# Kernel optimization log

Measured on AMD Instinct MI355X. Metric: run time of the kernel, lower is better.

Reference implementation:

```python
import jax, jax.numpy as jnp
import numpy as np

B = 256
N = 256


def setup_inputs() -> dict:
    key = jax.random.key(0)
    ks = jax.random.split(key, 6)
    X = jax.random.normal(ks[0], (B, N), dtype=jnp.float32)
    context = jax.random.normal(ks[1], (B, N), dtype=jnp.float32)
    W = jax.random.normal(ks[2], (N, N), dtype=jnp.float32) * 0.1
    scale = jnp.ones((1,), dtype=jnp.float32)
    A = jax.random.uniform(ks[3], (N, N), dtype=jnp.float32)
    cl_weight = jax.random.normal(ks[4], (N * N, N), dtype=jnp.float32) * 0.02
    cl_bias = jax.random.normal(ks[5], (N * N,), dtype=jnp.float32) * 0.02
    t = 3
    return {"X": X, "context": context, "W": W, "scale": scale, "A": A,
            "cl_weight": cl_weight, "cl_bias": cl_bias, "t": t}


def reference(X, context, W, scale, A, cl_weight, cl_bias, t):
    # context_L path: context-conditioned adjustment of W, shape [B, N, N]
    Bsz, n = X.shape
    adjust = (context @ cl_weight.T + cl_bias).reshape(Bsz, n, n)
    W_new = adjust + W  # broadcast [N,N] over batch
    # diag term: sum over rows i of (W_new @ A)[b, i, k] = einsum bij,jk->bk
    d = jnp.einsum('bij,jk->bk', W_new, A)
    eye = jnp.eye(n, dtype=X.dtype)
    L = d[:, :, None] * eye - W_new          # diag_embed(d) - W_new, [B,N,N]
    new_context = context * (t / (t + 1)) + X / (t + 1)
    L_T = scale * jnp.swapaxes(L, -1, -2)    # [B,N,N]
    update = jnp.einsum('bn,bnm->bm', X, L_T)  # matmul(X[...,None,:], L_T).squeeze()
    return (update, new_context)
```

## Files before the change

### kernel.cpp

```cpp
#include <hip/hip_runtime.h>

#define N 256
#define NN 65536

typedef __attribute__((ext_vector_type(8))) __bf16 bf16x8;
typedef __attribute__((ext_vector_type(4))) __bf16 bf16x4v;
typedef __attribute__((ext_vector_type(4))) float f32x4;

#define F_PART   0u
#define F_CSPART 2097152u
#define F_WSC    3145728u
#define F_CSB    3145984u
#define F_SFULL  3178752u
#define F_YADJ   3244288u
#define WS_FLOATS 3309824u

static __device__ __forceinline__ f32x4 mfma16(bf16x8 a, bf16x8 b, f32x4 c) {
  return __builtin_amdgcn_mfma_f32_16x16x32_bf16(a, b, c, 0, 0, 0);
}
static __device__ __forceinline__ bf16x4v pack4(float4 v) {
  bf16x4v r;
  r[0] = (__bf16)v.x; r[1] = (__bf16)v.y; r[2] = (__bf16)v.z; r[3] = (__bf16)v.w;
  return r;
}
static __device__ __forceinline__ bf16x8 pack8(float4 a, float4 b) {
  bf16x8 r;
  r[0] = (__bf16)a.x; r[1] = (__bf16)a.y; r[2] = (__bf16)a.z; r[3] = (__bf16)a.w;
  r[4] = (__bf16)b.x; r[5] = (__bf16)b.y; r[6] = (__bf16)b.z; r[7] = (__bf16)b.w;
  return r;
}

__global__ void __launch_bounds__(512) kbig(
    const float* __restrict__ X, const float* __restrict__ ctx,
    const float* __restrict__ W, const float* __restrict__ clb,
    const float* __restrict__ clw, float* __restrict__ ws)
{
  extern __shared__ char smem[];
  float* xl  = (float*)(smem + 65536);
  float* red = (float*)smem;
  const int t = threadIdx.x;
  const int mg = blockIdx.x >> 5, s = blockIdx.x & 31;
  const int m0 = mg * 16, n0 = s * 8;

  const int lane = t & 63, w = t >> 6;
  const int wb = w * 32;
  const int l15 = lane & 15, lhi = lane >> 4;
  const float4* clwf4 = (const float4*)clw;

  bf16x8 af[2][8];
#pragma unroll
  for (int i = 0; i < 2; ++i)
#pragma unroll
    for (int c = 0; c < 8; ++c) {
      const float4* p = (const float4*)(ctx + (wb + i * 16 + l15) * N +
                                        c * 32 + lhi * 8);
      af[i][c] = pack8(p[0], p[1]);
    }
  if (t < 256) {
    const float4* xp = (const float4*)(X + t * N + n0);
    const float4 x0 = xp[0], x1 = xp[1];
    xl[0 * 256 + t] = x0.x; xl[1 * 256 + t] = x0.y;
    xl[2 * 256 + t] = x0.z; xl[3 * 256 + t] = x0.w;
    xl[4 * 256 + t] = x1.x; xl[5 * 256 + t] = x1.y;
    xl[6 * 256 + t] = x1.z; xl[7 * 256 + t] = x1.w;
  }

  float4 cso = {0.f, 0.f, 0.f, 0.f};
  {
    float4 val[16];
#pragma unroll
    for (int r = 0; r < 16; ++r)
      val[r] = clwf4[(size_t)(m0 + r) * 16384 + n0 * 64 + t];
#pragma unroll
    for (int r = 0; r < 16; ++r) {
      cso.x += val[r].x; cso.y += val[r].y;
      cso.z += val[r].z; cso.w += val[r].w;
      *(bf16x4v*)(smem + r * 4096 + ((t * 8) ^ ((r & 7) << 4))) = pack4(val[r]);
    }
  }
  __syncthreads();

  const f32x4 zero = {0.f, 0.f, 0.f, 0.f};
  f32x4 acc[2];
  acc[0] = zero; acc[1] = zero;

#pragma unroll
  for (int n = 0; n < 8; ++n) {
    f32x4 h[2];
    h[0] = zero; h[1] = zero;
#pragma unroll
    for (int c = 0; c < 8; ++c) {
      const int kbyte = (c * 64 + lhi * 16) ^ ((l15 & 7) << 4);
      bf16x8 bf = *(const bf16x8*)(smem + l15 * 4096 + n * 512 + kbyte);
      h[0] = mfma16(af[0][c], bf, h[0]);
      h[1] = mfma16(af[1][c], bf, h[1]);
    }
#pragma unroll
    for (int r = 0; r < 4; ++r) {
      h[0][r] *= xl[n * 256 + wb + lhi * 4 + r];
      h[1][r] *= xl[n * 256 + wb + 16 + lhi * 4 + r];
      acc[0][r] += h[0][r];
      acc[1][r] += h[1][r];
    }
  }

  *(float4*)(ws + F_CSPART + mg * 65536u + s * 2048 + t * 4) = cso;

  const size_t base = (size_t)blockIdx.x * 4096;
#pragma unroll
  for (int i = 0; i < 2; ++i)
#pragma unroll
    for (int r = 0; r < 4; ++r)
      ws[F_PART + base + (size_t)(wb + i * 16 + lhi * 4 + r) * 16 + l15] =
          acc[i][r];

  if (mg == 0) {
    __syncthreads();
    if (t < 256) {
      const float4* wp = (const float4*)(W + t * N + s * 8);
      const float4* cp = (const float4*)(clb + t * N + s * 8);
      const float4 a0 = wp[0], a1 = wp[1], c0 = cp[0], c1 = cp[1];
      red[0 * 256 + t] = a0.x + c0.x; red[1 * 256 + t] = a0.y + c0.y;
      red[2 * 256 + t] = a0.z + c0.z; red[3 * 256 + t] = a0.w + c0.w;
      red[4 * 256 + t] = a1.x + c1.x; red[5 * 256 + t] = a1.y + c1.y;
      red[6 * 256 + t] = a1.z + c1.z; red[7 * 256 + t] = a1.w + c1.w;
    }
    __syncthreads();
    if (t < 64) {
      const int jj = t >> 3, seg = t & 7;
      float v = 0.f;
#pragma unroll
      for (int i = 0; i < 32; ++i) v += red[jj * 256 + seg * 32 + i];
      v += __shfl_xor(v, 1);
      v += __shfl_xor(v, 2);
      v += __shfl_xor(v, 4);
      if (seg == 0) ws[F_WSC + s * 8 + jj] = v;
    }
  }
}

__global__ void __launch_bounds__(256) kred(float* __restrict__ ws)
{
  const int o = blockIdx.x * 256 + threadIdx.x;
  const int b = o >> 8, m = o & 255;
  const int mgg = m >> 4, ml = m & 15;
  const size_t pb = F_PART + (size_t)(mgg * 32) * 4096 + (size_t)b * 16 + ml;
  float y = 0.f;
#pragma unroll
  for (int si = 0; si < 32; ++si)
    y += ws[pb + (size_t)si * 4096];
  ws[F_YADJ + o] = y;
  float cv = 0.f;
#pragma unroll
  for (int g = 0; g < 16; ++g)
    cv += ws[F_CSPART + g * 65536u + o];
  ((__bf16*)(ws + F_CSB))[o] = (__bf16)cv;
}

__global__ void __launch_bounds__(256) kred2(
    const float* __restrict__ ctx, float* __restrict__ ws)
{
  const int t = threadIdx.x, blk = blockIdx.x;
  const int b0 = (blk >> 3) * 32, j0 = (blk & 7) * 32;
  const int lane = t & 63, w = t >> 6;
  const int l15 = lane & 15, lhi = lane >> 4;
  const int wqb = (w >> 1) * 16, wqj = (w & 1) * 16;
  const char* csb = (const char*)(ws + F_CSB);

  f32x4 accq = {0.f, 0.f, 0.f, 0.f};
#pragma unroll
  for (int c = 0; c < 8; ++c) {
    const float4* p = (const float4*)(ctx + (b0 + wqb + l15) * N +
                                      c * 32 + lhi * 8);
    bf16x8 a = pack8(p[0], p[1]);
    bf16x8 b = *(const bf16x8*)(csb + (j0 + wqj + l15) * 512 +
                                c * 64 + lhi * 16);
    accq = mfma16(a, b, accq);
  }
  const int j = j0 + wqj + l15;
  const float wscv = ws[F_WSC + j];
#pragma unroll
  for (int r = 0; r < 4; ++r) {
    const int b = b0 + wqb + lhi * 4 + r;
    ws[F_SFULL + b * N + j] = accq[r] + wscv;
  }
}

__global__ void __launch_bounds__(256) kfin(
    const float* __restrict__ X, const float* __restrict__ ctx,
    const float* __restrict__ W, const float* __restrict__ clb,
    const float* __restrict__ A, const float* __restrict__ scale,
    const int* __restrict__ tptr, float* __restrict__ out,
    float* __restrict__ ws)
{
  extern __shared__ char smem[];
  const int t = threadIdx.x, blk = blockIdx.x;
  const int b0 = (blk >> 3) * 32, k0 = (blk & 7) * 32;
  {
    const int row = t >> 3, q = t & 7;
    const int sw = (row & 7) << 4;
    const float4* sp = (const float4*)(ws + F_SFULL + (b0 + row) * N);
    const float4* xp = (const float4*)(X + (b0 + row) * N);
    const float4* wp = (const float4*)(W + (k0 + row) * N);
    const float4* cp = (const float4*)(clb + (k0 + row) * N);
#pragma unroll
    for (int i = 0; i < 8; ++i) {
      const int f4 = q * 8 + i;
      const int off = row * 512 + ((f4 * 8) ^ sw);
      *(bf16x4v*)(smem + off) = pack4(sp[f4]);
      *(bf16x4v*)(smem + 16384 + off) = pack4(xp[f4]);
      const float4 wv = wp[f4], cv = cp[f4];
      float4 s2;
      s2.x = wv.x + cv.x; s2.y = wv.y + cv.y;
      s2.z = wv.z + cv.z; s2.w = wv.w + cv.w;
      *(bf16x4v*)(smem + 49152 + off) = pack4(s2);
    }
    const float4* ap = (const float4*)(A + t * N + k0);
    char* at = smem + 32768;
#pragma unroll
    for (int i = 0; i < 8; ++i) {
      const float4 v = ap[i];
      const int kk = i * 4;
      *(__bf16*)(at + (kk + 0) * 512 + ((t * 2) ^ (((kk + 0) & 7) << 4))) = (__bf16)v.x;
      *(__bf16*)(at + (kk + 1) * 512 + ((t * 2) ^ (((kk + 1) & 7) << 4))) = (__bf16)v.y;
      *(__bf16*)(at + (kk + 2) * 512 + ((t * 2) ^ (((kk + 2) & 7) << 4))) = (__bf16)v.z;
      *(__bf16*)(at + (kk + 3) * 512 + ((t * 2) ^ (((kk + 3) & 7) << 4))) = (__bf16)v.w;
    }
  }
  __syncthreads();
  const int lane = t & 63, w = t >> 6;
  const int l15 = lane & 15, lhi = lane >> 4;
  const int wqb = (w >> 1) * 16, wqk = (w & 1) * 16;
  const int swz = (l15 & 7) << 4;
  f32x4 accd = {0.f, 0.f, 0.f, 0.f}, accw = {0.f, 0.f, 0.f, 0.f};
#pragma unroll
  for (int c = 0; c < 8; ++c) {
    const int kb = c * 64 + lhi * 16;
    bf16x8 as  = *(const bf16x8*)(smem + (wqb + l15) * 512 + (kb ^ swz));
    bf16x8 aat = *(const bf16x8*)(smem + 32768 + (wqk + l15) * 512 + (kb ^ swz));
    bf16x8 ax  = *(const bf16x8*)(smem + 16384 + (wqb + l15) * 512 + (kb ^ swz));
    bf16x8 awc = *(const bf16x8*)(smem + 49152 + (wqk + l15) * 512 + (kb ^ swz));
    accd = mfma16(as, aat, accd);
    accw = mfma16(ax, awc, accw);
  }
  const float sc = scale[0];
  const float tf = (float)(*tptr);
  const float c1 = tf / (tf + 1.f), c2 = 1.f / (tf + 1.f);
#pragma unroll
  for (int r = 0; r < 4; ++r) {
    const int b = b0 + wqb + lhi * 4 + r, k = k0 + wqk + l15;
    const int idx = b * N + k;
    const float xv = X[idx];
    out[idx] = sc * (xv * accd[r] - accw[r] - ws[F_YADJ + idx]);
    out[NN + idx] = ctx[idx] * c1 + xv * c2;
  }
}

extern "C" void kernel_launch(void* const* d_in, const int* in_sizes, int n_in,
                              void* d_out, int out_size, void* d_ws, size_t ws_size,
                              hipStream_t stream)
{
  (void)in_sizes; (void)n_in; (void)out_size;
  const float* X     = (const float*)d_in[0];
  const float* ctx   = (const float*)d_in[1];
  const float* W     = (const float*)d_in[2];
  const float* scale = (const float*)d_in[3];
  const float* A     = (const float*)d_in[4];
  const float* clw   = (const float*)d_in[5];
  const float* clb   = (const float*)d_in[6];
  const int*   tptr  = (const int*)d_in[7];
  float* out = (float*)d_out;
  float* ws  = (float*)d_ws;

  if (ws_size < (size_t)WS_FLOATS * sizeof(float)) return;

  (void)hipFuncSetAttribute((const void*)kbig,
                            hipFuncAttributeMaxDynamicSharedMemorySize, 73728);
  (void)hipFuncSetAttribute((const void*)kfin,
                            hipFuncAttributeMaxDynamicSharedMemorySize, 65536);

  kbig<<<512, 512, 73728, stream>>>(X, ctx, W, clb, clw, ws);
  kred<<<256, 256, 0, stream>>>(ws);
  kred2<<<64, 256, 0, stream>>>(ctx, ws);
  kfin<<<64, 256, 65536, stream>>>(X, ctx, W, clb, A, scale, tptr, out, ws);
}
```

Baseline: 56.80 us.

## Pre-convert cl_weight to bf16 in a separate kernel before main GEMM

Adds a kcvt kernel that streams the fp32 cl_weight, writes a bf16 copy into the workspace and computes the column-sum partials. kbig then loads 16-byte bf16 vectors from that copy into shared memory instead of converting fp32 itself. The aim is to simplify kbig's load path and separate the conversion from the MFMA stage. In exchange it adds a kernel launch, an extra 32 MB write plus read-back of bf16 data, and a larger workspace.

```diff
diff --git a/kernel.cpp b/kernel.cpp
--- a/kernel.cpp
+++ b/kernel.cpp
@@ -7,13 +7,14 @@
 typedef __attribute__((ext_vector_type(4))) __bf16 bf16x4v;
 typedef __attribute__((ext_vector_type(4))) float f32x4;
 
-#define F_PART   0u
-#define F_CSPART 2097152u
-#define F_WSC    3145728u
-#define F_CSB    3145984u
-#define F_SFULL  3178752u
-#define F_YADJ   3244288u
-#define WS_FLOATS 3309824u
+#define F_CLWB   0u
+#define F_CSPART 8388608u
+#define F_PART   9437184u
+#define F_WSC    11534336u
+#define F_CSB    11534592u
+#define F_SFULL  11567360u
+#define F_YADJ   11632896u
+#define WS_FLOATS 11698432u
 
 static __device__ __forceinline__ f32x4 mfma16(bf16x8 a, bf16x8 b, f32x4 c) {
   return __builtin_amdgcn_mfma_f32_16x16x32_bf16(a, b, c, 0, 0, 0);
@@ -30,10 +31,27 @@
   return r;
 }
 
+__global__ void __launch_bounds__(256) kcvt(
+    const float* __restrict__ clw, float* __restrict__ ws)
+{
+  const int g = blockIdx.x * 256 + threadIdx.x;
+  const float4* in = (const float4*)clw;
+  bf16x4v* outb = (bf16x4v*)(ws + F_CLWB);
+  float4 cso = {0.f, 0.f, 0.f, 0.f};
+#pragma unroll
+  for (int i = 0; i < 16; ++i) {
+    const float4 v = in[(size_t)i * 262144 + g];
+    cso.x += v.x; cso.y += v.y; cso.z += v.z; cso.w += v.w;
+    outb[(size_t)i * 262144 + g] = pack4(v);
+  }
+  *(float4*)(ws + F_CSPART + (size_t)(g >> 14) * 65536 +
+             (size_t)(g & 16383) * 4) = cso;
+}
+
 __global__ void __launch_bounds__(512) kbig(
     const float* __restrict__ X, const float* __restrict__ ctx,
     const float* __restrict__ W, const float* __restrict__ clb,
-    const float* __restrict__ clw, float* __restrict__ ws)
+    float* __restrict__ ws)
 {
   extern __shared__ char smem[];
   float* xl  = (float*)(smem + 65536);
@@ -45,16 +63,25 @@
   const int lane = t & 63, w = t >> 6;
   const int wb = w * 32;
   const int l15 = lane & 15, lhi = lane >> 4;
-  const float4* clwf4 = (const float4*)clw;
+  const char* clwb = (const char*)(ws + F_CLWB);
+
+  const int p = t & 255, rh = t >> 8;
+  bf16x8 sval[8];
+#pragma unroll
+  for (int i = 0; i < 8; ++i) {
+    const int r = rh + 2 * i;
+    sval[i] = *(const bf16x8*)(
+        clwb + ((size_t)(m0 + r) * 65536 + (size_t)n0 * 256) * 2 + p * 16);
+  }
 
   bf16x8 af[2][8];
 #pragma unroll
   for (int i = 0; i < 2; ++i)
 #pragma unroll
     for (int c = 0; c < 8; ++c) {
-      const float4* p = (const float4*)(ctx + (wb + i * 16 + l15) * N +
-                                        c * 32 + lhi * 8);
-      af[i][c] = pack8(p[0], p[1]);
+      const float4* pc = (const float4*)(ctx + (wb + i * 16 + l15) * N +
+                                         c * 32 + lhi * 8);
+      af[i][c] = pack8(pc[0], pc[1]);
     }
   if (t < 256) {
     const float4* xp = (const float4*)(X + t * N + n0);
@@ -65,18 +92,10 @@
     xl[6 * 256 + t] = x1.z; xl[7 * 256 + t] = x1.w;
   }
 
-  float4 cso = {0.f, 0.f, 0.f, 0.f};
-  {
-    float4 val[16];
-#pragma unroll
-    for (int r = 0; r < 16; ++r)
-      val[r] = clwf4[(size_t)(m0 + r) * 16384 + n0 * 64 + t];
-#pragma unroll
-    for (int r = 0; r < 16; ++r) {
-      cso.x += val[r].x; cso.y += val[r].y;
-      cso.z += val[r].z; cso.w += val[r].w;
-      *(bf16x4v*)(smem + r * 4096 + ((t * 8) ^ ((r & 7) << 4))) = pack4(val[r]);
-    }
+#pragma unroll
+  for (int i = 0; i < 8; ++i) {
+    const int r = rh + 2 * i;
+    *(bf16x8*)(smem + r * 4096 + ((p * 16) ^ ((r & 7) << 4))) = sval[i];
   }
   __syncthreads();
 
@@ -90,8 +109,8 @@
     h[0] = zero; h[1] = zero;
 #pragma unroll
     for (int c = 0; c < 8; ++c) {
-      const int kbyte = (c * 64 + lhi * 16) ^ ((l15 & 7) << 4);
-      bf16x8 bf = *(const bf16x8*)(smem + l15 * 4096 + n * 512 + kbyte);
+      const int kbyte = (n * 512 + ((c * 64 + lhi * 16) ^ ((l15 & 7) << 4)));
+      bf16x8 bf = *(const bf16x8*)(smem + l15 * 4096 + kbyte);
       h[0] = mfma16(af[0][c], bf, h[0]);
       h[1] = mfma16(af[1][c], bf, h[1]);
     }
@@ -103,8 +122,6 @@
       acc[1][r] += h[1][r];
     }
   }
-
-  *(float4*)(ws + F_CSPART + mg * 65536u + s * 2048 + t * 4) = cso;
 
   const size_t base = (size_t)blockIdx.x * 4096;
 #pragma unroll
@@ -152,8 +169,8 @@
   ws[F_YADJ + o] = y;
   float cv = 0.f;
 #pragma unroll
-  for (int g = 0; g < 16; ++g)
-    cv += ws[F_CSPART + g * 65536u + o];
+  for (int q = 0; q < 16; ++q)
+    cv += ws[F_CSPART + q * 65536u + o];
   ((__bf16*)(ws + F_CSB))[o] = (__bf16)cv;
 }
 
@@ -279,7 +296,8 @@
   (void)hipFuncSetAttribute((const void*)kfin,
                             hipFuncAttributeMaxDynamicSharedMemorySize, 65536);
 
-  kbig<<<512, 512, 73728, stream>>>(X, ctx, W, clb, clw, ws);
+  kcvt<<<1024, 256, 0, stream>>>(clw, ws);
+  kbig<<<512, 512, 73728, stream>>>(X, ctx, W, clb, ws);
   kred<<<256, 256, 0, stream>>>(ws);
   kred2<<<64, 256, 0, stream>>>(ctx, ws);
   kfin<<<64, 256, 65536, stream>>>(X, ctx, W, clb, A, scale, tptr, out, ws);
```

New measurement: 69.58 us. 1.22x slower.
